# Kernel optimization log

Measured on AMD Instinct MI355X. Metric: run time of the kernel, lower is better.

## Reference

```python
import jax, jax.numpy as jnp
import numpy as np

N_NODES = 50000
N_EDGES = 800000
IN_DIM = 256
OUT_DIM = 64


def setup_inputs() -> dict:
    key = jax.random.key(0)
    k1, k2, k3, k4, k5 = jax.random.split(key, 5)
    h = jax.random.normal(k1, (N_NODES, IN_DIM), dtype=jnp.float32)
    # fc: Linear(in_dim, out_dim, bias=False) -> weight shape [out_dim, in_dim]
    W_fc = jax.random.normal(k2, (OUT_DIM, IN_DIM), dtype=jnp.float32) / np.sqrt(IN_DIM)
    # attn_fc: Linear(2*out_dim, 1, bias=False) -> weight shape [1, 2*out_dim]
    W_attn = jax.random.normal(k3, (1, 2 * OUT_DIM), dtype=jnp.float32) / np.sqrt(2 * OUT_DIM)
    src = jax.random.randint(k4, (N_EDGES,), 0, N_NODES, dtype=jnp.int64 if jax.config.read('jax_enable_x64') else jnp.int32).astype(jnp.int32)
    dst = jax.random.randint(k5, (N_EDGES,), 0, N_NODES, dtype=jnp.int32)
    return {"h": h, "W_fc": W_fc, "W_attn": W_attn, "src": src, "dst": dst}


def reference(h, W_fc, W_attn, src, dst):
    # z = self.fc(h)
    z = h @ W_fc.T                              # [N, D]
    # edge_attention: e = leaky_relu(attn_fc(cat(z_src, z_dst)))
    z_src = z[src]                              # [E, D] gather
    z_dst = z[dst]                              # [E, D] gather
    z2 = jnp.concatenate([z_src, z_dst], axis=1)  # [E, 2D]
    e = jax.nn.leaky_relu(z2 @ W_attn.T)[:, 0]  # [E], torch default slope 0.01
    # reduce_func: segment softmax over incoming edges per dst node
    n = h.shape[0]
    m = jax.ops.segment_max(e, dst, num_segments=n)        # [N] per-node max
    e_exp = jnp.exp(e - m[dst])                             # [E] stable exp
    denom = jax.ops.segment_sum(e_exp, dst, num_segments=n)  # [N]
    alpha = e_exp / jnp.maximum(denom, 1e-16)[dst]          # [E]
    # h' = sum_j alpha_ij * z_j
    out = jax.ops.segment_sum(alpha[:, None] * z_src, dst, num_segments=n)  # [N, D]
    return out
```

## Files before the change

kernel.cpp:

```cpp
#include <hip/hip_runtime.h>

#define N_NODES 50000
#define N_EDGES 800000
#define IN_DIM  256
#define OUT_DIM 64
#define BINW    128
#define NBINS   512
#define NBINS_USED ((N_NODES + BINW - 1) / BINW)
#define PB      112
#define CH4     ((N_EDGES / 4 + PB - 1) / PB)
#define NB_GEMM ((N_NODES + 63) / 64)
#define GRID_FUSED 896

typedef _Float16 f16;
typedef __attribute__((ext_vector_type(2))) __fp16 hf16x2;
typedef __attribute__((ext_vector_type(4))) _Float16 f16x4;
typedef __attribute__((ext_vector_type(8))) _Float16 f16x8;
typedef __attribute__((ext_vector_type(4))) float f32x4;


__global__ __launch_bounds__(256) void k_prep(const float* __restrict__ W,
                                              f16* __restrict__ Wh,
                                              int* __restrict__ binCount) {
    int idx = blockIdx.x * 256 + threadIdx.x;
    if (idx < (OUT_DIM * IN_DIM) / 4) {
        float4 v = ((const float4*)W)[idx];
        f16x4 p = { (f16)v.x, (f16)v.y, (f16)v.z, (f16)v.w };
        ((f16x4*)Wh)[idx] = p;
    }
    if (idx < NBINS) binCount[idx] = 0;
}

__global__ __launch_bounds__(256) void k_fused(const float* __restrict__ h,
                                               const f16* __restrict__ Wh,
                                               const float* __restrict__ Wa,
                                               const int* __restrict__ dst,
                                               f16* __restrict__ z,
                                               float* __restrict__ a_src,
                                               float* __restrict__ a_dst,
                                               int* __restrict__ binCount,
                                               int* __restrict__ base) {
    __shared__ int hist[NBINS];
    const int g = blockIdx.x;
    const int t = threadIdx.x;

    if ((g & 7) == 7) {
        const int pb = g >> 3;
        for (int b = t; b < NBINS; b += 256) hist[b] = 0;
        __syncthreads();
        const int s4 = pb * CH4;
        const int e4 = min(s4 + CH4, N_EDGES / 4);
        for (int i4 = s4 + t; i4 < e4; i4 += 256) {
            int4 dv = ((const int4*)dst)[i4];
            atomicAdd(&hist[dv.x >> 7], 1);
            atomicAdd(&hist[dv.y >> 7], 1);
            atomicAdd(&hist[dv.z >> 7], 1);
            atomicAdd(&hist[dv.w >> 7], 1);
        }
        __syncthreads();
        for (int b = t; b < NBINS; b += 256) {
            int c = hist[b];
            if (c) base[pb * NBINS + b] = atomicAdd(&binCount[b], c);
        }
        return;
    }

    const int gemm_id = g - (g >> 3);
    if (gemm_id >= NB_GEMM) return;

    const int row0  = gemm_id * 64;
    const int lane  = t & 63;
    const int wid   = t >> 6;
    const int cl    = lane & 15;
    const int khalf = lane >> 4;

    const int arow = row0 + wid * 16 + cl;
    const bool rok = arow < N_NODES;
    const float* hrow = h + (size_t)arow * IN_DIM;

    f32x4 acc[4] = {};

    #pragma unroll 4
    for (int kc = 0; kc < IN_DIM; kc += 32) {
        const int k0 = kc + khalf * 8;
        float4 va = make_float4(0.f, 0.f, 0.f, 0.f);
        float4 vb = make_float4(0.f, 0.f, 0.f, 0.f);
        if (rok) {
            va = *(const float4*)&hrow[k0];
            vb = *(const float4*)&hrow[k0 + 4];
        }
        union { hf16x2 h2[4]; f16x8 h8; } ua;
        ua.h2[0] = __builtin_amdgcn_cvt_pkrtz(va.x, va.y);
        ua.h2[1] = __builtin_amdgcn_cvt_pkrtz(va.z, va.w);
        ua.h2[2] = __builtin_amdgcn_cvt_pkrtz(vb.x, vb.y);
        ua.h2[3] = __builtin_amdgcn_cvt_pkrtz(vb.z, vb.w);
        f16x8 a = ua.h8;
        #pragma unroll
        for (int ct = 0; ct < 4; ++ct) {
            const int col = ct * 16 + cl;
            f16x8 b = *(const f16x8*)&Wh[col * 256 + k0];
            acc[ct] = __builtin_amdgcn_mfma_f32_16x16x32_f16(a, b, acc[ct], 0, 0, 0);
        }
    }

    const int rbase = row0 + wid * 16 + khalf * 4;
    #pragma unroll
    for (int ct = 0; ct < 4; ++ct) {
        #pragma unroll
        for (int r = 0; r < 4; ++r) {
            int row = rbase + r;
            if (row < N_NODES)
                z[(size_t)row * OUT_DIM + ct * 16 + cl] = (f16)acc[ct][r];
        }
    }

    float wa1[4], wa2[4];
    #pragma unroll
    for (int ct = 0; ct < 4; ++ct) {
        wa1[ct] = Wa[ct * 16 + cl];
        wa2[ct] = Wa[64 + ct * 16 + cl];
    }
    #pragma unroll
    for (int r = 0; r < 4; ++r) {
        float s1 = 0.f, s2 = 0.f;
        #pragma unroll
        for (int ct = 0; ct < 4; ++ct) {
            s1 += acc[ct][r] * wa1[ct];
            s2 += acc[ct][r] * wa2[ct];
        }
        #pragma unroll
        for (int off = 1; off < 16; off <<= 1) {
            s1 += __shfl_xor(s1, off);
            s2 += __shfl_xor(s2, off);
        }
        int row = rbase + r;
        if (cl == 0 && row < N_NODES) {
            a_src[row] = s1;
            a_dst[row] = s2;
        }
    }
}

__global__ __launch_bounds__(256) void k_place(const int* __restrict__ src,
                                               const int* __restrict__ dst,
                                               const int* __restrict__ binCount,
                                               const int* __restrict__ base,
                                               int* __restrict__ ebuf) {
    __shared__ int cursor[NBINS];
    const int pb = blockIdx.x;
    const int t  = threadIdx.x;

    if (t < 64) {
        int vals[8]; int run = 0;
        #pragma unroll
        for (int i = 0; i < 8; ++i) { int c = binCount[t * 8 + i]; vals[i] = run; run += c; }
        int incl = run;
        #pragma unroll
        for (int off = 1; off < 64; off <<= 1) {
            int u = __shfl_up(incl, off);
            if (t >= off) incl += u;
        }
        const int lex = incl - run;
        #pragma unroll
        for (int i = 0; i < 8; ++i) cursor[t * 8 + i] = lex + vals[i];
    }
    __syncthreads();
    for (int b = t; b < NBINS; b += 256) cursor[b] += base[pb * NBINS + b];
    __syncthreads();

    const int s4 = pb * CH4;
    const int e4 = min(s4 + CH4, N_EDGES / 4);
    for (int i4 = s4 + t; i4 < e4; i4 += 256) {
        int4 dv = ((const int4*)dst)[i4];
        int4 sv = ((const int4*)src)[i4];
        int slot;
        slot = atomicAdd(&cursor[dv.x >> 7], 1); ebuf[slot] = (sv.x << 7) | (dv.x & 127);
        slot = atomicAdd(&cursor[dv.y >> 7], 1); ebuf[slot] = (sv.y << 7) | (dv.y & 127);
        slot = atomicAdd(&cursor[dv.z >> 7], 1); ebuf[slot] = (sv.z << 7) | (dv.z & 127);
        slot = atomicAdd(&cursor[dv.w >> 7], 1); ebuf[slot] = (sv.w << 7) | (dv.w & 127);
    }
}

__global__ __launch_bounds__(256) void k_place2(const int* __restrict__ ebuf,
                                                const int* __restrict__ binCount,
                                                int* __restrict__ csr_src,
                                                int* __restrict__ rowptr) {
    __shared__ int cnt[BINW];
    __shared__ int cur[BINW];
    __shared__ int sh_estart;
    const int b  = blockIdx.x;
    const int t  = threadIdx.x;
    const int node0 = b * BINW;
    const int ecnt  = binCount[b];

    if (t < 64) {
        int partial = 0;
        for (int i = t; i < b; i += 64) partial += binCount[i];
        #pragma unroll
        for (int off = 32; off; off >>= 1) partial += __shfl_xor(partial, off);
        if (t == 0) sh_estart = partial;
    }
    if (t < BINW) cnt[t] = 0;
    __syncthreads();
    const int estart = sh_estart;

    for (int i = t; i < ecnt; i += 256)
        atomicAdd(&cnt[ebuf[estart + i] & (BINW - 1)], 1);
    __syncthreads();

    if (t < 64) {
        int v0 = cnt[t], v1 = cnt[t + 64];
        int i0 = v0;
        #pragma unroll
        for (int off = 1; off < 64; off <<= 1) {
            int u = __shfl_up(i0, off);
            if (t >= off) i0 += u;
        }
        int tot0 = __shfl(i0, 63);
        int i1 = v1;
        #pragma unroll
        for (int off = 1; off < 64; off <<= 1) {
            int u = __shfl_up(i1, off);
            if (t >= off) i1 += u;
        }
        int e0 = i0 - v0;
        int e1 = tot0 + i1 - v1;
        cur[t]      = e0;
        cur[t + 64] = e1;
        if (node0 + t <= N_NODES)      rowptr[node0 + t]      = estart + e0;
        if (node0 + t + 64 <= N_NODES) rowptr[node0 + t + 64] = estart + e1;
    }
    __syncthreads();

    for (int i = t; i < ecnt; i += 256) {
        int pk = ebuf[estart + i];
        int ld = pk & (BINW - 1);
        int p  = atomicAdd(&cur[ld], 1);
        csr_src[estart + p] = pk >> 7;
    }
}

__global__ __launch_bounds__(256) void k_aggregate(const int* __restrict__ rowptr,
                                                   const int* __restrict__ csr_src,
                                                   const float* __restrict__ a_src,
                                                   const float* __restrict__ a_dst,
                                                   const f16* __restrict__ z,
                                                   float* __restrict__ out) {
    __shared__ float2 buf[4][64];
    const int wid  = threadIdx.x >> 6;
    const int lane = threadIdx.x & 63;
    const int node = blockIdx.x * 4 + wid;
    if (node >= N_NODES) return;

    const int beg = rowptr[node];
    const int end = rowptr[node + 1];
    const int deg = end - beg;
    const float adst = a_dst[node];

    const int grp = lane >> 3;
    const int cl  = lane & 7;
    float dn = 0.0f;
    float acc8[8] = {0.f, 0.f, 0.f, 0.f, 0.f, 0.f, 0.f, 0.f};

    if (deg <= 64) {
        int s = 0;
        float w = 0.0f;
        if (lane < deg) {
            s = csr_src[beg + lane];
            float u = a_src[s] + adst;
            u = u > 0.0f ? u : 0.01f * u;
            w = __expf(u);
        }
        dn = w;

        buf[wid][lane] = make_float2(w, __int_as_float(s));
        __builtin_amdgcn_wave_barrier();

        const int kmax = (deg + 7) & ~7;
        for (int k = 0; k < kmax; k += 8) {
            float2 p = buf[wid][k + grp];
            int   sk = __float_as_int(p.y);
            float wk = p.x;
            f16x8 zv = *(const f16x8*)&z[(size_t)sk * OUT_DIM + cl * 8];
            #pragma unroll
            for (int j = 0; j < 8; ++j)
                acc8[j] = fmaf(wk, (float)zv[j], acc8[j]);
        }
    } else {
        float mx = -INFINITY;
        for (int j = beg + lane; j < end; j += 64) {
            int s = csr_src[j];
            float u = a_src[s] + adst;
            u = u > 0.0f ? u : 0.01f * u;
            mx = fmaxf(mx, u);
        }
        #pragma unroll
        for (int off = 32; off; off >>= 1) mx = fmaxf(mx, __shfl_xor(mx, off));

        for (int base_ = beg; base_ < end; base_ += 64) {
            int rem = end - base_; if (rem > 64) rem = 64;
            int s = 0; float w = 0.0f;
            if (lane < rem) {
                s = csr_src[base_ + lane];
                float u = a_src[s] + adst;
                u = u > 0.0f ? u : 0.01f * u;
                w = __expf(u - mx);
            }
            dn += w;
            __builtin_amdgcn_wave_barrier();
            buf[wid][lane] = make_float2(w, __int_as_float(s));
            __builtin_amdgcn_wave_barrier();

            const int kmax = (rem + 7) & ~7;
            for (int k = 0; k < kmax; k += 8) {
                float2 p = buf[wid][k + grp];
                int   sk = __float_as_int(p.y);
                float wk = p.x;
                f16x8 zv = *(const f16x8*)&z[(size_t)sk * OUT_DIM + cl * 8];
                #pragma unroll
                for (int j = 0; j < 8; ++j)
                    acc8[j] = fmaf(wk, (float)zv[j], acc8[j]);
            }
            __builtin_amdgcn_wave_barrier();
        }
    }

    #pragma unroll
    for (int off = 32; off; off >>= 1) dn += __shfl_xor(dn, off);
    #pragma unroll
    for (int off = 8; off < 64; off <<= 1) {
        #pragma unroll
        for (int j = 0; j < 8; ++j)
            acc8[j] += __shfl_xor(acc8[j], off);
    }

    if (lane < 8) {
        float inv = 1.0f / fmaxf(dn, 1e-16f);
        float4 o0 = make_float4(acc8[0] * inv, acc8[1] * inv, acc8[2] * inv, acc8[3] * inv);
        float4 o1 = make_float4(acc8[4] * inv, acc8[5] * inv, acc8[6] * inv, acc8[7] * inv);
        *(float4*)&out[(size_t)node * OUT_DIM + lane * 8]     = o0;
        *(float4*)&out[(size_t)node * OUT_DIM + lane * 8 + 4] = o1;
    }
}


extern "C" void kernel_launch(void* const* d_in, const int* in_sizes, int n_in,
                              void* d_out, int out_size, void* d_ws, size_t ws_size,
                              hipStream_t stream) {
    const float* h      = (const float*)d_in[0];
    const float* W_fc   = (const float*)d_in[1];
    const float* W_attn = (const float*)d_in[2];
    const int*   src    = (const int*)d_in[3];
    const int*   dst    = (const int*)d_in[4];
    float* out = (float*)d_out;

    f16*   z        = (f16*)d_ws;
    f16*   Wh       = z + (size_t)N_NODES * OUT_DIM;
    float* a_src    = (float*)(Wh + OUT_DIM * IN_DIM);
    float* a_dst    = a_src + N_NODES;
    int*   binCount = (int*)(a_dst + N_NODES);
    int*   rowptr   = binCount + NBINS;
    int*   base     = rowptr + (N_NODES + 1);
    int*   ebuf     = base + PB * NBINS;
    int*   csr_src  = ebuf + N_EDGES;

    k_prep<<<16, 256, 0, stream>>>(W_fc, Wh, binCount);
    k_fused<<<GRID_FUSED, 256, 0, stream>>>(h, Wh, W_attn, dst, z, a_src, a_dst, binCount, base);
    k_place<<<PB, 256, 0, stream>>>(src, dst, binCount, base, ebuf);
    k_place2<<<NBINS_USED, 256, 0, stream>>>(ebuf, binCount, csr_src, rowptr);
    k_aggregate<<<(N_NODES + 3) / 4, 256, 0, stream>>>(rowptr, csr_src, a_src, a_dst, z, out);
}
```

Baseline: 79.39 us.

## Precompute edge softmax weights in CSR build and pack with source index

The edge attention weight exp(leaky_relu(a_src+a_dst)) is now computed in k_place2 while the CSR is scattered, and stored as an fp16 value packed into the low 16 bits next to the source index in the high 16 bits. k_aggregate for degree ≤64 then reads one word per edge and no longer gathers a_src randomly or evaluates exp, which takes a dependent random load off its critical path. The GEMM also clamps out-of-range rows instead of branching on loads. Risks: the 16-bit source field only holds indices up to 65535, the weight loses precision in fp16, and the unnormalized exp can overflow fp16 when there is no max subtraction.

```diff
diff --git a/kernel.cpp b/kernel.cpp
--- a/kernel.cpp
+++ b/kernel.cpp
@@ -17,6 +17,19 @@
 typedef __attribute__((ext_vector_type(4))) _Float16 f16x4;
 typedef __attribute__((ext_vector_type(8))) _Float16 f16x8;
 typedef __attribute__((ext_vector_type(4))) float f32x4;
+
+__device__ __forceinline__ unsigned int pack_sw(int s, float w) {
+    f16 hw = (f16)w;
+    unsigned short us;
+    __builtin_memcpy(&us, &hw, 2);
+    return ((unsigned int)s << 16) | us;
+}
+__device__ __forceinline__ float unpack_w(unsigned int e) {
+    unsigned short us = (unsigned short)(e & 0xffffu);
+    f16 hw;
+    __builtin_memcpy(&hw, &us, 2);
+    return (float)hw;
+}
 
 
 __global__ __launch_bounds__(256) void k_prep(const float* __restrict__ W,
@@ -74,8 +87,8 @@
     const int cl    = lane & 15;
     const int khalf = lane >> 4;
 
-    const int arow = row0 + wid * 16 + cl;
-    const bool rok = arow < N_NODES;
+    int arow = row0 + wid * 16 + cl;
+    if (arow >= N_NODES) arow = N_NODES - 1;
     const float* hrow = h + (size_t)arow * IN_DIM;
 
     f32x4 acc[4] = {};
@@ -83,12 +96,8 @@
     #pragma unroll 4
     for (int kc = 0; kc < IN_DIM; kc += 32) {
         const int k0 = kc + khalf * 8;
-        float4 va = make_float4(0.f, 0.f, 0.f, 0.f);
-        float4 vb = make_float4(0.f, 0.f, 0.f, 0.f);
-        if (rok) {
-            va = *(const float4*)&hrow[k0];
-            vb = *(const float4*)&hrow[k0 + 4];
-        }
+        float4 va = *(const float4*)&hrow[k0];
+        float4 vb = *(const float4*)&hrow[k0 + 4];
         union { hf16x2 h2[4]; f16x8 h8; } ua;
         ua.h2[0] = __builtin_amdgcn_cvt_pkrtz(va.x, va.y);
         ua.h2[1] = __builtin_amdgcn_cvt_pkrtz(va.z, va.w);
@@ -183,10 +192,13 @@
 
 __global__ __launch_bounds__(256) void k_place2(const int* __restrict__ ebuf,
                                                 const int* __restrict__ binCount,
-                                                int* __restrict__ csr_src,
+                                                const float* __restrict__ a_src,
+                                                const float* __restrict__ a_dst,
+                                                int* __restrict__ csr,
                                                 int* __restrict__ rowptr) {
     __shared__ int cnt[BINW];
     __shared__ int cur[BINW];
+    __shared__ float adl[BINW];
     __shared__ int sh_estart;
     const int b  = blockIdx.x;
     const int t  = threadIdx.x;
@@ -200,7 +212,11 @@
         for (int off = 32; off; off >>= 1) partial += __shfl_xor(partial, off);
         if (t == 0) sh_estart = partial;
     }
-    if (t < BINW) cnt[t] = 0;
+    if (t < BINW) {
+        cnt[t] = 0;
+        int gd = node0 + t;
+        adl[t] = (gd < N_NODES) ? a_dst[gd] : 0.f;
+    }
     __syncthreads();
     const int estart = sh_estart;
 
@@ -235,18 +251,22 @@
     for (int i = t; i < ecnt; i += 256) {
         int pk = ebuf[estart + i];
         int ld = pk & (BINW - 1);
+        int s  = pk >> 7;
+        float u = a_src[s] + adl[ld];
+        u = u > 0.f ? u : 0.01f * u;
+        float w = __expf(u);
         int p  = atomicAdd(&cur[ld], 1);
-        csr_src[estart + p] = pk >> 7;
+        csr[estart + p] = (int)pack_sw(s, w);
     }
 }
 
 __global__ __launch_bounds__(256) void k_aggregate(const int* __restrict__ rowptr,
-                                                   const int* __restrict__ csr_src,
+                                                   const int* __restrict__ csr,
                                                    const float* __restrict__ a_src,
                                                    const float* __restrict__ a_dst,
                                                    const f16* __restrict__ z,
                                                    float* __restrict__ out) {
-    __shared__ float2 buf[4][64];
+    __shared__ unsigned int buf[4][64];
     const int wid  = threadIdx.x >> 6;
     const int lane = threadIdx.x & 63;
     const int node = blockIdx.x * 4 + wid;
@@ -255,7 +275,6 @@
     const int beg = rowptr[node];
     const int end = rowptr[node + 1];
     const int deg = end - beg;
-    const float adst = a_dst[node];
 
     const int grp = lane >> 3;
     const int cl  = lane & 7;
@@ -263,33 +282,28 @@
     float acc8[8] = {0.f, 0.f, 0.f, 0.f, 0.f, 0.f, 0.f, 0.f};
 
     if (deg <= 64) {
-        int s = 0;
-        float w = 0.0f;
-        if (lane < deg) {
-            s = csr_src[beg + lane];
-            float u = a_src[s] + adst;
-            u = u > 0.0f ? u : 0.01f * u;
-            w = __expf(u);
-        }
-        dn = w;
-
-        buf[wid][lane] = make_float2(w, __int_as_float(s));
+        unsigned int e = 0;
+        if (lane < deg) e = (unsigned int)csr[beg + lane];
+        dn = unpack_w(e);
+
+        buf[wid][lane] = e;
         __builtin_amdgcn_wave_barrier();
 
         const int kmax = (deg + 7) & ~7;
         for (int k = 0; k < kmax; k += 8) {
-            float2 p = buf[wid][k + grp];
-            int   sk = __float_as_int(p.y);
-            float wk = p.x;
+            unsigned int pe = buf[wid][k + grp];
+            int   sk = (int)(pe >> 16);
+            float wk = unpack_w(pe);
             f16x8 zv = *(const f16x8*)&z[(size_t)sk * OUT_DIM + cl * 8];
             #pragma unroll
             for (int j = 0; j < 8; ++j)
                 acc8[j] = fmaf(wk, (float)zv[j], acc8[j]);
         }
     } else {
+        const float adst = a_dst[node];
         float mx = -INFINITY;
         for (int j = beg + lane; j < end; j += 64) {
-            int s = csr_src[j];
+            int s = (int)(((unsigned int)csr[j]) >> 16);
             float u = a_src[s] + adst;
             u = u > 0.0f ? u : 0.01f * u;
             mx = fmaxf(mx, u);
@@ -301,21 +315,21 @@
             int rem = end - base_; if (rem > 64) rem = 64;
             int s = 0; float w = 0.0f;
             if (lane < rem) {
-                s = csr_src[base_ + lane];
+                s = (int)(((unsigned int)csr[base_ + lane]) >> 16);
                 float u = a_src[s] + adst;
                 u = u > 0.0f ? u : 0.01f * u;
                 w = __expf(u - mx);
             }
             dn += w;
             __builtin_amdgcn_wave_barrier();
-            buf[wid][lane] = make_float2(w, __int_as_float(s));
+            buf[wid][lane] = pack_sw(s, w);
             __builtin_amdgcn_wave_barrier();
 
             const int kmax = (rem + 7) & ~7;
             for (int k = 0; k < kmax; k += 8) {
-                float2 p = buf[wid][k + grp];
-                int   sk = __float_as_int(p.y);
-                float wk = p.x;
+                unsigned int pe = buf[wid][k + grp];
+                int   sk = (int)(pe >> 16);
+                float wk = unpack_w(pe);
                 f16x8 zv = *(const f16x8*)&z[(size_t)sk * OUT_DIM + cl * 8];
                 #pragma unroll
                 for (int j = 0; j < 8; ++j)
@@ -362,11 +376,11 @@
     int*   rowptr   = binCount + NBINS;
     int*   base     = rowptr + (N_NODES + 1);
     int*   ebuf     = base + PB * NBINS;
-    int*   csr_src  = ebuf + N_EDGES;
+    int*   csr      = ebuf + N_EDGES;
 
     k_prep<<<16, 256, 0, stream>>>(W_fc, Wh, binCount);
     k_fused<<<GRID_FUSED, 256, 0, stream>>>(h, Wh, W_attn, dst, z, a_src, a_dst, binCount, base);
     k_place<<<PB, 256, 0, stream>>>(src, dst, binCount, base, ebuf);
-    k_place2<<<NBINS_USED, 256, 0, stream>>>(ebuf, binCount, csr_src, rowptr);
-    k_aggregate<<<(N_NODES + 3) / 4, 256, 0, stream>>>(rowptr, csr_src, a_src, a_dst, z, out);
-}
+    k_place2<<<NBINS_USED, 256, 0, stream>>>(ebuf, binCount, a_src, a_dst, csr, rowptr);
+    k_aggregate<<<(N_NODES + 3) / 4, 256, 0, stream>>>(rowptr, csr, a_src, a_dst, z, out);
+}
```

Result: no change. 80.03 us (+0.8%).
